# Kernel tuning notes

Measured on AMD Instinct MI355X. Metric: run time of the kernel, lower is better.

The kernel has to match this reference:

```python
import jax, jax.numpy as jnp
import numpy as np

B, T, DIM, H, HD = 1, 4096, 1024, 8, 128
ATTN_SCALE = 0.12


def _rms_norm(x):
    # F.rms_norm with default eps = finfo(dtype).eps, no learned weight
    eps = jnp.asarray(jnp.finfo(x.dtype).eps, x.dtype)
    return x * jax.lax.rsqrt(jnp.mean(x * x, axis=-1, keepdims=True) + eps)


def _rotary(x):
    # x: [B, T, H, D]; half-rotary: last D/2 freqs are zero (identity)
    t, d = x.shape[1], x.shape[-1]
    freqs = (1.0 / 1024.0) ** jnp.linspace(0.0, 1.0, d // 4, dtype=jnp.float32)
    freqs = jnp.concatenate([freqs, jnp.zeros(d // 4, dtype=jnp.float32)])
    theta = jnp.arange(t, dtype=jnp.float32)[:, None] * freqs[None, :]  # [T, D/2]
    cos = jnp.cos(theta)[None, :, None, :]
    sin = jnp.sin(theta)[None, :, None, :]
    x1, x2 = jnp.split(x.astype(jnp.float32), 2, axis=-1)
    y = jnp.concatenate([x1 * cos + x2 * sin, -x1 * sin + x2 * cos], axis=-1)
    return y.astype(x.dtype)


def setup_inputs() -> dict:
    key = jax.random.key(0)
    k1, k2, k3, k4, k5 = jax.random.split(key, 5)
    std = 0.5 * DIM ** -0.5
    bound = (3.0 ** 0.5) * std
    x = jax.random.normal(k1, (B, T, DIM), dtype=jnp.float32)
    ve = jax.random.normal(k2, (B, T, DIM), dtype=jnp.float32)
    qkv_w = jax.random.uniform(k3, (3, H * HD, DIM), dtype=jnp.float32,
                               minval=-bound, maxval=bound)
    lambdas = jnp.array([0.5, 0.5], dtype=jnp.float32)
    # c_proj is zero-initialized in the source; use small random weights so the
    # output (and gradients) are non-trivial for correctness testing
    c_proj_w = jax.random.normal(k4, (DIM, H * HD), dtype=jnp.float32) * 0.02
    docs = jnp.sort(jax.random.randint(k5, (T,), 0, 8, dtype=jnp.int32))
    return {"x": x, "ve": ve, "qkv_w": qkv_w, "lambdas": lambdas,
            "c_proj_w": c_proj_w, "docs": docs}


def reference(x, ve, qkv_w, lambdas, c_proj_w, docs):
    b, t, _ = x.shape
    w = qkv_w.reshape(3 * H * HD, -1)              # [3*hdim, dim]
    qkv = (x @ w.T).reshape(b, t, 3, H, HD)        # chunk(3, dim=-2) == axis 2 here
    q, k, v = qkv[:, :, 0], qkv[:, :, 1], qkv[:, :, 2]
    q, k = _rms_norm(q), _rms_norm(k)
    q, k = _rotary(q), _rotary(k)
    v = lambdas[0] * v + lambdas[1] * ve.reshape(v.shape)
    # doc-causal mask: attend within the same document, causally
    i = jnp.arange(t)
    mask = (i[:, None] >= i[None, :]) & (docs[:, None] == docs[None, :])  # [T, T]
    scores = jnp.einsum('bihd,bjhd->bhij', q, k) * ATTN_SCALE
    scores = jnp.where(mask[None, None], scores, -jnp.inf)
    p = jax.nn.softmax(scores, axis=-1)
    y = jnp.einsum('bhij,bjhd->bihd', p, v).reshape(b, t, H * HD)
    return y @ c_proj_w.T
```

## Files before the change

kernel.cpp:

```cpp
#include <hip/hip_runtime.h>
#include <hip/hip_bf16.h>
#include <cstdint>

typedef __attribute__((ext_vector_type(8))) short sh8;
typedef __attribute__((ext_vector_type(4))) float f4;
typedef __attribute__((ext_vector_type(16))) float f16v;

#define T_SEQ 4096
#define DIMN  1024
#define NH    8
#define HDIM  128
#define NQKV  3072
#define ATTN_SCALE 0.12f

__device__ __forceinline__ ushort f2bf(float x) {
  __hip_bfloat16 b = __float2bfloat16(x);
  return *reinterpret_cast<ushort*>(&b);
}
__device__ __forceinline__ float bf2f(ushort u) {
  uint v = ((uint)u) << 16;
  float f;
  __builtin_memcpy(&f, &v, 4);
  return f;
}

#define GLDS16(g, l) \
  __builtin_amdgcn_global_load_lds((const __attribute__((address_space(1))) void*)(g), \
                                   (__attribute__((address_space(3))) void*)(l), 16, 0, 0)

template <int N>
__device__ __forceinline__ void wait_vmcnt() {
  if constexpr (N == 0)      asm volatile("s_waitcnt vmcnt(0)" ::: "memory");
  else if constexpr (N == 4) asm volatile("s_waitcnt vmcnt(4)" ::: "memory");
  else if constexpr (N == 8) asm volatile("s_waitcnt vmcnt(8)" ::: "memory");
  __builtin_amdgcn_sched_barrier(0);
}
#define BAR __builtin_amdgcn_s_barrier()

__global__ __launch_bounds__(256) void k_prep(const float* __restrict__ x,
                                              const float* __restrict__ qw,
                                              const float* __restrict__ cw,
                                              ushort* __restrict__ xb, ushort* __restrict__ wb,
                                              ushort* __restrict__ cbuf,
                                              const int* __restrict__ docs, int* __restrict__ dstart) {
  const int b = blockIdx.x;
  if (b < 8192) {
    const int i = b * 256 + threadIdx.x;
    const float* src;
    ushort* dst;
    int j;
    if (i < 1048576)       { src = x;  dst = xb;   j = i; }
    else if (i < 1835008)  { src = qw; dst = wb;   j = i - 1048576; }
    else                   { src = cw; dst = cbuf; j = i - 1835008; }
    float4 v = reinterpret_cast<const float4*>(src)[j];
    ushort4 o;
    o.x = f2bf(v.x); o.y = f2bf(v.y); o.z = f2bf(v.z); o.w = f2bf(v.w);
    reinterpret_cast<ushort4*>(dst)[j] = o;
  } else {
    const int i = (b - 8192) * 256 + threadIdx.x;
    if (i < T_SEQ) {
      int d = docs[i];
      int lo = 0, hi = i;
      while (lo < hi) { int mid = (lo + hi) >> 1; if (docs[mid] < d) lo = mid + 1; else hi = mid; }
      dstart[i] = lo;
    }
  }
}

__global__ __launch_bounds__(512, 2) void k_gemm32(const ushort* __restrict__ A,
                                                   const ushort* __restrict__ B,
                                                   ushort* __restrict__ C,
                                                   int N, int K) {
  __shared__ ushort lds[2][512 * 64];
  const int tid = threadIdx.x;
  const int lane = tid & 63;
  const int w = tid >> 6;
  const int l5 = lane >> 5;
  const int lr32 = lane & 31;
  const int wave_m = w >> 2, wave_n = w & 3;

  const int bid = blockIdx.x;
  const int s = (bid & 7) * 32 + (bid >> 3);
  const int m0 = ((s >> 5) * 4 + ((s >> 3) & 3)) * 128;
  const int n0 = (s & 7) * 384;

  f16v acc[2][3];
#pragma unroll
  for (int i = 0; i < 2; ++i)
#pragma unroll
    for (int j = 0; j < 3; ++j)
#pragma unroll
      for (int r = 0; r < 16; ++r) acc[i][j][r] = 0.f;

  const int NT = K >> 6;

  auto STAGE4 = [&](int buf, int t, int ug) {
    const int k0 = t << 6;
#pragma unroll
    for (int uu = 0; uu < 4; ++uu) {
      const int u = ug * 4 + uu;
      const int row = u * 64 + (tid >> 3);
      const int c = (tid & 7) ^ (row & 7);
      const ushort* src = (u < 2) ? (A + (size_t)(m0 + row) * K + k0 + c * 8)
                                  : (B + (size_t)(n0 + row - 128) * K + k0 + c * 8);
      GLDS16(src, (char*)&lds[buf][0] + u * 8192 + w * 1024);
    }
  };

  STAGE4(0, 0, 0); STAGE4(0, 0, 1);
  wait_vmcnt<0>();
  BAR;

  int cur = 0;
  for (int t = 0; t < NT; ++t) {
    const bool more = (t + 1) < NT;
    const char* bb = (const char*)&lds[cur][0];

#define RD_FRAGS(ks, a, b)                                                        \
    _Pragma("unroll") for (int mt = 0; mt < 2; ++mt) {                            \
      const int row = wave_m * 64 + mt * 32 + lr32;                               \
      a[mt] = *(const sh8*)(bb + row * 128 + ((((ks) * 2 + l5) ^ (row & 7)) * 16));\
    }                                                                             \
    _Pragma("unroll") for (int nt = 0; nt < 3; ++nt) {                            \
      const int row = 128 + wave_n * 96 + nt * 32 + lr32;                         \
      b[nt] = *(const sh8*)(bb + row * 128 + ((((ks) * 2 + l5) ^ (row & 7)) * 16));\
    }

#define MFMA6(a, b)                                                               \
    __builtin_amdgcn_s_setprio(1);                                                \
    _Pragma("unroll") for (int mt = 0; mt < 2; ++mt)                              \
    _Pragma("unroll") for (int nt = 0; nt < 3; ++nt)                              \
      acc[mt][nt] = __builtin_amdgcn_mfma_f32_32x32x16_bf16(a[mt], b[nt],         \
                                                            acc[mt][nt], 0, 0, 0);\
    __builtin_amdgcn_s_setprio(0);

    {
      sh8 a[2], b[3];
      RD_FRAGS(0, a, b)
      if (more) STAGE4(cur ^ 1, t + 1, 0);
      MFMA6(a, b)
    }
    {
      sh8 a[2], b[3];
      RD_FRAGS(1, a, b)
      if (more) STAGE4(cur ^ 1, t + 1, 1);
      MFMA6(a, b)
    }
    BAR;
    {
      sh8 a[2], b[3];
      RD_FRAGS(2, a, b)
      MFMA6(a, b)
    }
    if (more) wait_vmcnt<4>();
    {
      sh8 a[2], b[3];
      RD_FRAGS(3, a, b)
      MFMA6(a, b)
    }
    if (more) wait_vmcnt<0>();
    BAR;
    cur ^= 1;
  }
#undef RD_FRAGS
#undef MFMA6

#pragma unroll
  for (int mt = 0; mt < 2; ++mt)
#pragma unroll
    for (int nt = 0; nt < 3; ++nt) {
      const int gcol = n0 + wave_n * 96 + nt * 32 + lr32;
#pragma unroll
      for (int r = 0; r < 16; ++r) {
        const int grow = m0 + wave_m * 64 + mt * 32 + (r & 3) + 8 * (r >> 2) + 4 * l5;
        C[(size_t)grow * N + gcol] = f2bf(acc[mt][nt][r]);
      }
    }
}

__global__ __launch_bounds__(256) void k_gemm2(const ushort* __restrict__ A,
                                               const ushort* __restrict__ B,
                                               float* __restrict__ C,
                                               int N, int K, int gx) {
  constexpr int BM = 128, BN = 128;
  constexpr int CHA = BM * 4;
  constexpr int TILEB = (BM + BN) * 64;

  __shared__ __attribute__((aligned(16))) char lds[3 * TILEB];

  const int tid = threadIdx.x;
  const int lane = tid & 63;
  const int w = tid >> 6;
  const int l5 = lane >> 5;
  const int lr32 = lane & 31;
  const int wm = w >> 1, wn = w & 1;

  const int nwg = gridDim.x;
  const int nb = (blockIdx.x & 7) * (nwg >> 3) + (blockIdx.x >> 3);
  const int m0 = (nb / gx) * BM;
  const int n0 = (nb % gx) * BN;

  f16v acc[2][2];
#pragma unroll
  for (int i = 0; i < 2; ++i)
#pragma unroll
    for (int j = 0; j < 2; ++j)
#pragma unroll
      for (int r = 0; r < 16; ++r) acc[i][j][r] = 0.f;

  const int NT = K >> 5;

  auto STAGE = [&](int t, int buf) {
    const int k0 = t << 5;
#pragma unroll
    for (int l = 0; l < 4; ++l) {
      const int cb = (l * 4 + w) * 64;
      const int ch = cb + lane;
      const ushort* src;
      if (ch < CHA) {
        const int row = ch >> 2;
        const int cs = (ch & 3) ^ ((row >> 1) & 3);
        src = A + (size_t)(m0 + row) * K + k0 + cs * 8;
      } else {
        const int c2 = ch - CHA;
        const int row = c2 >> 2;
        const int cs = (c2 & 3) ^ ((row >> 1) & 3);
        src = B + (size_t)(n0 + row) * K + k0 + cs * 8;
      }
      GLDS16(src, lds + buf * TILEB + cb * 16);
    }
  };

  STAGE(0, 0);
  STAGE(1, 1);
  wait_vmcnt<4>();
  BAR;

  int bufc = 0;
  for (int t = 0; t < NT; ++t) {
    const bool more = (t + 2) < NT;
    if (more) STAGE(t + 2, bufc == 0 ? 2 : (bufc == 1 ? 0 : 1));

    const char* bb = lds + bufc * TILEB;
#pragma unroll
    for (int ks = 0; ks < 2; ++ks) {
      sh8 a[2], b[2];
#pragma unroll
      for (int mt = 0; mt < 2; ++mt) {
        const int row = wm * 64 + mt * 32 + lr32;
        a[mt] = *(const sh8*)(bb + row * 64 + (((ks * 2 + l5) ^ ((row >> 1) & 3)) * 16));
      }
#pragma unroll
      for (int nt = 0; nt < 2; ++nt) {
        const int row = wn * 64 + nt * 32 + lr32;
        b[nt] = *(const sh8*)(bb + BM * 64 + row * 64 + (((ks * 2 + l5) ^ ((row >> 1) & 3)) * 16));
      }
      __builtin_amdgcn_s_setprio(1);
#pragma unroll
      for (int mt = 0; mt < 2; ++mt)
#pragma unroll
        for (int nt = 0; nt < 2; ++nt)
          acc[mt][nt] = __builtin_amdgcn_mfma_f32_32x32x16_bf16(a[mt], b[nt], acc[mt][nt], 0, 0, 0);
      __builtin_amdgcn_s_setprio(0);
    }

    if (more) wait_vmcnt<4>();
    else      wait_vmcnt<0>();
    BAR;
    bufc = bufc == 2 ? 0 : bufc + 1;
  }

#pragma unroll
  for (int mt = 0; mt < 2; ++mt)
#pragma unroll
    for (int nt = 0; nt < 2; ++nt) {
      const int gcol = n0 + wn * 64 + nt * 32 + lr32;
#pragma unroll
      for (int r = 0; r < 16; ++r) {
        const int grow = m0 + wm * 64 + mt * 32 + (r & 3) + 8 * (r >> 2) + 4 * l5;
        __builtin_nontemporal_store(acc[mt][nt][r], &C[(size_t)grow * N + gcol]);
      }
    }
}

__global__ __launch_bounds__(256) void k_fuse(const ushort* __restrict__ qkvb,
                                              const float* __restrict__ ve,
                                              const float* __restrict__ lam,
                                              ushort* __restrict__ qh, ushort* __restrict__ kh,
                                              ushort* __restrict__ vh) {
  const int pair = blockIdx.x * 4 + (threadIdx.x >> 6);
  const int t = pair >> 3, h = pair & 7;
  const int l = threadIdx.x & 63;
  const ushort* base = qkvb + (size_t)t * NQKV + h * HDIM + 2 * l;
  uint qu = *reinterpret_cast<const uint*>(base);
  uint ku = *reinterpret_cast<const uint*>(base + 1024);
  uint vu = *reinterpret_cast<const uint*>(base + 2048);
  float q0 = bf2f((ushort)qu), q1 = bf2f((ushort)(qu >> 16));
  float k0 = bf2f((ushort)ku), k1 = bf2f((ushort)(ku >> 16));
  float v0 = bf2f((ushort)vu), v1 = bf2f((ushort)(vu >> 16));
  float sq = q0 * q0 + q1 * q1, sk = k0 * k0 + k1 * k1;
#pragma unroll
  for (int m = 1; m < 64; m <<= 1) { sq += __shfl_xor(sq, m); sk += __shfl_xor(sk, m); }
  const float eps = 1.1920928955078125e-07f;
  float rq = rsqrtf(sq * (1.f / 128.f) + eps);
  float rk = rsqrtf(sk * (1.f / 128.f) + eps);
  q0 *= rq; q1 *= rq; k0 *= rk; k1 *= rk;
  float c0 = 1.f, s0 = 0.f, c1 = 1.f, s1 = 0.f;
  if ((l & 31) < 16) {
    const int f0 = 2 * (l & 31);
    float fr0 = exp2f(-10.f * (float)f0 * (1.f / 31.f));
    float fr1 = exp2f(-10.f * (float)(f0 + 1) * (1.f / 31.f));
    sincosf((float)t * fr0, &s0, &c0);
    sincosf((float)t * fr1, &s1, &c1);
  }
  float qx0 = __shfl_xor(q0, 32), qx1 = __shfl_xor(q1, 32);
  float kx0 = __shfl_xor(k0, 32), kx1 = __shfl_xor(k1, 32);
  const float sgn = (l < 32) ? 1.f : -1.f;
  float qr0 = q0 * c0 + sgn * qx0 * s0;
  float qr1 = q1 * c1 + sgn * qx1 * s1;
  float kr0 = k0 * c0 + sgn * kx0 * s0;
  float kr1 = k1 * c1 + sgn * kx1 * s1;
  const float l0 = lam[0], l1 = lam[1];
  float2 vev = *reinterpret_cast<const float2*>(ve + (size_t)t * DIMN + h * HDIM + 2 * l);
  float vr0 = l0 * v0 + l1 * vev.x;
  float vr1 = l0 * v1 + l1 * vev.y;
  const size_t o = ((size_t)h * T_SEQ + t) * HDIM + 2 * l;
  *reinterpret_cast<uint*>(qh + o) = (uint)f2bf(qr0) | ((uint)f2bf(qr1) << 16);
  *reinterpret_cast<uint*>(kh + o) = (uint)f2bf(kr0) | ((uint)f2bf(kr1) << 16);
  *reinterpret_cast<uint*>(vh + o) = (uint)f2bf(vr0) | ((uint)f2bf(vr1) << 16);
}

__global__ __launch_bounds__(256) void k_vt(const ushort* __restrict__ vh, ushort* __restrict__ vt) {
  const int tb = blockIdx.x, db = blockIdx.y, h = blockIdx.z;
  __shared__ ushort L[64][68];
  const int tid = threadIdx.x;
  const int t0 = tb * 64, d0 = db * 64;
  const size_t ib = ((size_t)h * T_SEQ + t0) * HDIM + d0;
#pragma unroll
  for (int p = 0; p < 4; ++p) {
    const int row = p * 16 + (tid >> 4);
    const int c4 = (tid & 15) * 4;
    ushort4 v = *reinterpret_cast<const ushort4*>(vh + ib + (size_t)row * HDIM + c4);
    *reinterpret_cast<ushort4*>(&L[row][c4]) = v;
  }
  __syncthreads();
  const size_t ob = ((size_t)h * HDIM + d0) * T_SEQ + t0;
#pragma unroll
  for (int p = 0; p < 4; ++p) {
    const int drow = p * 16 + (tid >> 4);
    const int t4 = (tid & 15) * 4;
    ushort4 v;
    v.x = L[t4 + 0][drow]; v.y = L[t4 + 1][drow];
    v.z = L[t4 + 2][drow]; v.w = L[t4 + 3][drow];
    *reinterpret_cast<ushort4*>(vt + ob + (size_t)drow * T_SEQ + t4) = v;
  }
}

__global__ __launch_bounds__(256) void k_attn(const ushort* __restrict__ qh,
                                              const ushort* __restrict__ kh,
                                              const ushort* __restrict__ vt,
                                              const int* __restrict__ doc_start,
                                              ushort* __restrict__ y) {
  const int h  = blockIdx.x;
  const int qb = blockIdx.y;
  const int q0 = qb * 64;
  const int tid  = threadIdx.x;
  const int wave = tid >> 6;
  const int lane = tid & 63;
  const int lr = lane & 15, lg = lane >> 4;

  __shared__ ushort Ks[2][64 * 128];
  __shared__ ushort Vs[2][128 * 64];
  __shared__ ushort Ps[4][16 * 64];

  const ushort* Kg = kh + (size_t)h * T_SEQ * HDIM;
  const ushort* Vg = vt + (size_t)h * HDIM * T_SEQ;

  const int i_me = q0 + wave * 16 + lr;
  sh8 qf[4];
  {
    const ushort* qp = qh + ((size_t)h * T_SEQ + i_me) * HDIM + lg * 8;
#pragma unroll
    for (int c = 0; c < 4; ++c) qf[c] = *reinterpret_cast<const sh8*>(qp + c * 32);
  }
  const int ds_me = doc_start[i_me];
  const int ds_hi = doc_start[q0 + 63];
  const int kb0   = doc_start[q0] >> 6;

  const f4 fzero = {0.f, 0.f, 0.f, 0.f};
  f4 o_acc[8];
#pragma unroll
  for (int i = 0; i < 8; ++i) o_acc[i] = fzero;
  float m_me = -1e30f, l_me = 0.f;

  auto STAGE = [&](int b, int k0) {
#pragma unroll
    for (int p = 0; p < 4; ++p) {
      const int c = p * 256 + tid;
      const int row = c >> 4, cc = c & 15;
      GLDS16(Kg + (size_t)(k0 + row) * HDIM + (cc ^ (row & 7)) * 8,
             &Ks[b][(p * 256 + wave * 64) * 8]);
    }
#pragma unroll
    for (int p = 0; p < 4; ++p) {
      const int c = p * 256 + tid;
      const int d = c >> 3, cc = c & 7;
      GLDS16(Vg + (size_t)d * T_SEQ + k0 + (cc ^ (d & 7)) * 8,
             &Vs[b][(p * 256 + wave * 64) * 8]);
    }
  };

  int cur = 0;
  STAGE(0, kb0 * 64);

  const int sw = (lr & 7) << 4;

  for (int kb = kb0; kb <= qb; ++kb) {
    const int k0 = kb * 64;
    __syncthreads();
    if (kb < qb) STAGE(cur ^ 1, k0 + 64);

    const char* Kb = (const char*)&Ks[cur][0];
    const char* Vb = (const char*)&Vs[cur][0];
    char* Pw = (char*)&Ps[wave][0];

    f4 sacc[4];
#pragma unroll
    for (int jt = 0; jt < 4; ++jt) sacc[jt] = fzero;
#pragma unroll
    for (int jt = 0; jt < 4; ++jt)
#pragma unroll
      for (int c = 0; c < 4; ++c) {
        sh8 kf = *reinterpret_cast<const sh8*>(Kb + (jt * 16 + lr) * 256 + ((c * 64 + lg * 16) ^ sw));
        sacc[jt] = __builtin_amdgcn_mfma_f32_16x16x32_bf16(kf, qf[c], sacc[jt], 0, 0, 0);
      }

    const bool fullblk = (kb < qb) && (ds_hi <= k0);
    float p[4][4];
#pragma unroll
    for (int jt = 0; jt < 4; ++jt)
#pragma unroll
      for (int r = 0; r < 4; ++r) {
        float s = sacc[jt][r] * ATTN_SCALE;
        const int j = k0 + jt * 16 + lg * 4 + r;
        bool valid = fullblk || ((j <= i_me) && (j >= ds_me));
        p[jt][r] = valid ? s : -1e30f;
      }
    float tm = -1e30f;
#pragma unroll
    for (int jt = 0; jt < 4; ++jt) {
      float a = fmaxf(p[jt][0], p[jt][1]), b = fmaxf(p[jt][2], p[jt][3]);
      tm = fmaxf(tm, fmaxf(a, b));
    }
    tm = fmaxf(tm, __shfl_xor(tm, 16));
    tm = fmaxf(tm, __shfl_xor(tm, 32));
    const float mnew = fmaxf(m_me, tm);
    const float sc = __expf(m_me - mnew);
    m_me = mnew;
    float rs = 0.f;
#pragma unroll
    for (int jt = 0; jt < 4; ++jt)
#pragma unroll
      for (int r = 0; r < 4; ++r) {
        float pv = __expf(p[jt][r] - mnew);
        p[jt][r] = pv;
        rs += pv;
      }
    rs += __shfl_xor(rs, 16);
    rs += __shfl_xor(rs, 32);
    l_me = l_me * sc + rs;

#pragma unroll
    for (int jt = 0; jt < 4; ++jt) {
      uint2 u;
      u.x = (uint)f2bf(p[jt][0]) | ((uint)f2bf(p[jt][1]) << 16);
      u.y = (uint)f2bf(p[jt][2]) | ((uint)f2bf(p[jt][3]) << 16);
      *reinterpret_cast<uint2*>(Pw + lr * 128 + ((jt * 32 + lg * 8) ^ sw)) = u;
    }

    float sco[4];
#pragma unroll
    for (int rr = 0; rr < 4; ++rr) sco[rr] = __shfl(sc, lg * 4 + rr);
#pragma unroll
    for (int dt = 0; dt < 8; ++dt)
#pragma unroll
      for (int rr = 0; rr < 4; ++rr) o_acc[dt][rr] *= sco[rr];

#pragma unroll
    for (int ks = 0; ks < 2; ++ks) {
      sh8 pa = *reinterpret_cast<const sh8*>(Pw + lr * 128 + ((ks * 64 + lg * 16) ^ sw));
#pragma unroll
      for (int dt = 0; dt < 8; ++dt) {
        sh8 vf = *reinterpret_cast<const sh8*>(Vb + (dt * 16 + lr) * 128 + ((ks * 64 + lg * 16) ^ sw));
        o_acc[dt] = __builtin_amdgcn_mfma_f32_16x16x32_bf16(pa, vf, o_acc[dt], 0, 0, 0);
      }
    }

    __builtin_amdgcn_s_barrier();
    cur ^= 1;
  }

  float lo[4];
#pragma unroll
  for (int rr = 0; rr < 4; ++rr) lo[rr] = __shfl(l_me, lg * 4 + rr);
#pragma unroll
  for (int dt = 0; dt < 8; ++dt)
#pragma unroll
    for (int rr = 0; rr < 4; ++rr) {
      const int trow = q0 + wave * 16 + lg * 4 + rr;
      y[(size_t)trow * DIMN + h * HDIM + dt * 16 + lr] = f2bf(o_acc[dt][rr] / lo[rr]);
    }
}

extern "C" void kernel_launch(void* const* d_in, const int* in_sizes, int n_in,
                              void* d_out, int out_size, void* d_ws, size_t ws_size,
                              hipStream_t stream) {
  const float* x    = (const float*)d_in[0];
  const float* ve   = (const float*)d_in[1];
  const float* qkvw = (const float*)d_in[2];
  const float* lam  = (const float*)d_in[3];
  const float* cpw  = (const float*)d_in[4];
  const int*   docs = (const int*)d_in[5];
  float* out = (float*)d_out;
  char* ws = (char*)d_ws;

  ushort* qkvb = (ushort*)(ws);
  ushort* xb   = (ushort*)(ws + (24ull << 20));
  ushort* wb   = (ushort*)(ws + (32ull << 20));
  ushort* cb   = (ushort*)(ws + (38ull << 20));
  ushort* qh   = (ushort*)(ws + (40ull << 20));
  ushort* kh   = (ushort*)(ws + (48ull << 20));
  ushort* vh   = (ushort*)(ws + (56ull << 20));
  ushort* vt   = (ushort*)(ws + (64ull << 20));
  ushort* yb   = (ushort*)(ws + (72ull << 20));
  int*  dstart = (int*)(ws + (80ull << 20));

  k_prep<<<8192 + 16, 256, 0, stream>>>(x, qkvw, cpw, xb, wb, cb, docs, dstart);

  k_gemm32<<<256, 512, 0, stream>>>(xb, wb, qkvb, NQKV, DIMN);

  k_fuse<<<T_SEQ * NH / 4, 256, 0, stream>>>(qkvb, ve, lam, qh, kh, vh);
  k_vt<<<dim3(T_SEQ / 64, HDIM / 64, NH), 256, 0, stream>>>(vh, vt);

  k_attn<<<dim3(NH, T_SEQ / 64), 256, 0, stream>>>(qh, kh, vt, dstart, yb);

  k_gemm2<<<256, 256, 0, stream>>>(yb, cb, out, DIMN, DIMN, DIMN / 128);
}
```

Baseline: 101.2 us.

## Deepen GEMM pipelines to four LDS stages with smaller K tiles

```diff
diff --git a/kernel.cpp b/kernel.cpp
--- a/kernel.cpp
+++ b/kernel.cpp
@@ -71,7 +71,7 @@
                                                    const ushort* __restrict__ B,
                                                    ushort* __restrict__ C,
                                                    int N, int K) {
-  __shared__ ushort lds[2][512 * 64];
+  __shared__ ushort lds[4][512 * 32];
   const int tid = threadIdx.x;
   const int lane = tid & 63;
   const int w = tid >> 6;
@@ -92,78 +92,56 @@
 #pragma unroll
       for (int r = 0; r < 16; ++r) acc[i][j][r] = 0.f;
 
-  const int NT = K >> 6;
-
-  auto STAGE4 = [&](int buf, int t, int ug) {
-    const int k0 = t << 6;
-#pragma unroll
-    for (int uu = 0; uu < 4; ++uu) {
-      const int u = ug * 4 + uu;
-      const int row = u * 64 + (tid >> 3);
-      const int c = (tid & 7) ^ (row & 7);
-      const ushort* src = (u < 2) ? (A + (size_t)(m0 + row) * K + k0 + c * 8)
-                                  : (B + (size_t)(n0 + row - 128) * K + k0 + c * 8);
-      GLDS16(src, (char*)&lds[buf][0] + u * 8192 + w * 1024);
+  const int NT = K >> 5;
+
+  auto STAGE = [&](int t, int buf) {
+    const int k0 = t << 5;
+#pragma unroll
+    for (int l = 0; l < 4; ++l) {
+      const int idx = l * 512 + tid;
+      const int row = idx >> 2;
+      const int c = (idx & 3) ^ ((row >> 1) & 3);
+      const ushort* src = (row < 128 ? A + (size_t)(m0 + row) * K
+                                     : B + (size_t)(n0 + row - 128) * K) + k0 + c * 8;
+      GLDS16(src, (char*)&lds[buf][0] + (l * 512 + w * 64) * 16);
     }
   };
 
-  STAGE4(0, 0, 0); STAGE4(0, 0, 1);
-  wait_vmcnt<0>();
+  STAGE(0, 0); STAGE(1, 1); STAGE(2, 2);
+  wait_vmcnt<8>();
   BAR;
 
-  int cur = 0;
   for (int t = 0; t < NT; ++t) {
-    const bool more = (t + 1) < NT;
-    const char* bb = (const char*)&lds[cur][0];
-
-#define RD_FRAGS(ks, a, b)                                                        \
-    _Pragma("unroll") for (int mt = 0; mt < 2; ++mt) {                            \
-      const int row = wave_m * 64 + mt * 32 + lr32;                               \
-      a[mt] = *(const sh8*)(bb + row * 128 + ((((ks) * 2 + l5) ^ (row & 7)) * 16));\
-    }                                                                             \
-    _Pragma("unroll") for (int nt = 0; nt < 3; ++nt) {                            \
-      const int row = 128 + wave_n * 96 + nt * 32 + lr32;                         \
-      b[nt] = *(const sh8*)(bb + row * 128 + ((((ks) * 2 + l5) ^ (row & 7)) * 16));\
-    }
-
-#define MFMA6(a, b)                                                               \
-    __builtin_amdgcn_s_setprio(1);                                                \
-    _Pragma("unroll") for (int mt = 0; mt < 2; ++mt)                              \
-    _Pragma("unroll") for (int nt = 0; nt < 3; ++nt)                              \
-      acc[mt][nt] = __builtin_amdgcn_mfma_f32_32x32x16_bf16(a[mt], b[nt],         \
-                                                            acc[mt][nt], 0, 0, 0);\
-    __builtin_amdgcn_s_setprio(0);
-
-    {
+    if (t + 3 < NT) STAGE(t + 3, (t + 3) & 3);
+
+    const char* bb = (const char*)&lds[t & 3][0];
+#pragma unroll
+    for (int ks = 0; ks < 2; ++ks) {
       sh8 a[2], b[3];
-      RD_FRAGS(0, a, b)
-      if (more) STAGE4(cur ^ 1, t + 1, 0);
-      MFMA6(a, b)
-    }
-    {
-      sh8 a[2], b[3];
-      RD_FRAGS(1, a, b)
-      if (more) STAGE4(cur ^ 1, t + 1, 1);
-      MFMA6(a, b)
-    }
+#pragma unroll
+      for (int mt = 0; mt < 2; ++mt) {
+        const int row = wave_m * 64 + mt * 32 + lr32;
+        a[mt] = *(const sh8*)(bb + row * 64 + (((ks * 2 + l5) ^ ((row >> 1) & 3)) * 16));
+      }
+#pragma unroll
+      for (int nt = 0; nt < 3; ++nt) {
+        const int row = 128 + wave_n * 96 + nt * 32 + lr32;
+        b[nt] = *(const sh8*)(bb + row * 64 + (((ks * 2 + l5) ^ ((row >> 1) & 3)) * 16));
+      }
+      __builtin_amdgcn_s_setprio(1);
+#pragma unroll
+      for (int mt = 0; mt < 2; ++mt)
+#pragma unroll
+        for (int nt = 0; nt < 3; ++nt)
+          acc[mt][nt] = __builtin_amdgcn_mfma_f32_32x32x16_bf16(a[mt], b[nt], acc[mt][nt], 0, 0, 0);
+      __builtin_amdgcn_s_setprio(0);
+    }
+
+    if (t + 3 < NT)      wait_vmcnt<8>();
+    else if (t + 2 < NT) wait_vmcnt<4>();
+    else if (t + 1 < NT) wait_vmcnt<0>();
     BAR;
-    {
-      sh8 a[2], b[3];
-      RD_FRAGS(2, a, b)
-      MFMA6(a, b)
-    }
-    if (more) wait_vmcnt<4>();
-    {
-      sh8 a[2], b[3];
-      RD_FRAGS(3, a, b)
-      MFMA6(a, b)
-    }
-    if (more) wait_vmcnt<0>();
-    BAR;
-    cur ^= 1;
-  }
-#undef RD_FRAGS
-#undef MFMA6
+  }
 
 #pragma unroll
   for (int mt = 0; mt < 2; ++mt)
@@ -186,7 +164,7 @@
   constexpr int CHA = BM * 4;
   constexpr int TILEB = (BM + BN) * 64;
 
-  __shared__ __attribute__((aligned(16))) char lds[3 * TILEB];
+  __shared__ __attribute__((aligned(16))) char lds[4 * TILEB];
 
   const int tid = threadIdx.x;
   const int lane = tid & 63;
@@ -231,17 +209,14 @@
     }
   };
 
-  STAGE(0, 0);
-  STAGE(1, 1);
-  wait_vmcnt<4>();
+  STAGE(0, 0); STAGE(1, 1); STAGE(2, 2);
+  wait_vmcnt<8>();
   BAR;
 
-  int bufc = 0;
   for (int t = 0; t < NT; ++t) {
-    const bool more = (t + 2) < NT;
-    if (more) STAGE(t + 2, bufc == 0 ? 2 : (bufc == 1 ? 0 : 1));
-
-    const char* bb = lds + bufc * TILEB;
+    if (t + 3 < NT) STAGE(t + 3, (t + 3) & 3);
+
+    const char* bb = lds + (t & 3) * TILEB;
 #pragma unroll
     for (int ks = 0; ks < 2; ++ks) {
       sh8 a[2], b[2];
@@ -264,10 +239,10 @@
       __builtin_amdgcn_s_setprio(0);
     }
 
-    if (more) wait_vmcnt<4>();
-    else      wait_vmcnt<0>();
+    if (t + 3 < NT)      wait_vmcnt<8>();
+    else if (t + 2 < NT) wait_vmcnt<4>();
+    else if (t + 1 < NT) wait_vmcnt<0>();
     BAR;
-    bufc = bufc == 2 ? 0 : bufc + 1;
   }
 
 #pragma unroll
```

After: 104.9 us. +3.6%, slower.
